# Performance work log

Hardware: AMD Instinct MI355X
Metric: run time of the kernel (lower is better)

Reference implementation:

```python
import jax, jax.numpy as jnp
import numpy as np

N_NODES = 100000


def gcn_conv(x, W, b, src, dst, n):
    # x: [N, Fin], W: [Fin, Fout]. GCNConv: D^-1/2 (A+I) D^-1/2 (X W) + b
    h = x @ W  # [N, Fout]
    ones = jnp.ones_like(dst, dtype=h.dtype)
    deg = jax.ops.segment_sum(ones, dst, num_segments=n)  # in-degree incl self-loops
    dinv = jnp.where(deg > 0, jax.lax.rsqrt(deg), 0.0)
    norm = dinv[src] * dinv[dst]  # [E]
    msg = h[src] * norm[:, None]  # gather + scale
    out = jax.ops.segment_sum(msg, dst, num_segments=n)  # scatter-add
    return out + b


def setup_inputs() -> dict:
    key = jax.random.key(0)
    k1, k2, k3, k4 = jax.random.split(key, 4)
    F_IN, H, C, E = 512, 256, 40, 3200000
    x = jax.random.normal(k1, (N_NODES, F_IN), dtype=jnp.float32)
    # glorot-ish init
    W1 = jax.random.normal(k2, (F_IN, H), dtype=jnp.float32) * (1.0 / np.sqrt(F_IN))
    b1 = jnp.zeros((H,), dtype=jnp.float32)
    W2 = jax.random.normal(k3, (H, C), dtype=jnp.float32) * (1.0 / np.sqrt(H))
    b2 = jnp.zeros((C,), dtype=jnp.float32)
    edge_index = jax.random.randint(k4, (2, E), 0, N_NODES, dtype=jnp.int64)
    return {"x": x, "W1": W1, "b1": b1, "W2": W2, "b2": b2, "edge_index": edge_index}


def reference(x, W1, b1, W2, b2, edge_index):
    n = x.shape[0]
    # add self-loops (PyG GCNConv default add_self_loops=True)
    loop = jnp.arange(n, dtype=edge_index.dtype)
    src = jnp.concatenate([edge_index[0], loop])
    dst = jnp.concatenate([edge_index[1], loop])
    h = gcn_conv(x, W1, b1, src, dst, n)
    h = jax.nn.relu(h)
    # F.dropout(training=self.training): identity in eval mode
    h = gcn_conv(h, W2, b2, src, dst, n)
    return jax.nn.log_softmax(h, axis=1)
```

## Files before the change

kernel.cpp:

```cpp
#include <hip/hip_runtime.h>
#include <stdint.h>

typedef __attribute__((ext_vector_type(8))) short bf16x8;
typedef __attribute__((ext_vector_type(4))) float f32x4;
typedef __attribute__((ext_vector_type(4))) int i32x4;

__device__ __forceinline__ unsigned short f2bf(float f) {
    unsigned int u = __float_as_uint(f);
    u += 0x7FFFu + ((u >> 16) & 1u);
    return (unsigned short)(u >> 16);
}
__device__ __forceinline__ float bf2f(unsigned short s) {
    return __uint_as_float(((unsigned int)s) << 16);
}
__device__ __forceinline__ unsigned char fp8_enc(float f) {
    f = fminf(fmaxf(f, -448.f), 448.f);
    unsigned int u = __float_as_uint(f * 0x1p-120f);
    u += 0x7FFFFu + ((u >> 20) & 1u);
    return (unsigned char)(((u >> 20) & 0x7F) | ((u >> 24) & 0x80));
}

#define SLAB_CAP 5120

__global__ __launch_bounds__(256) void k_bscatter(const int* __restrict__ src,
                                                  const int* __restrict__ dst, int E,
                                                  int* __restrict__ bcnt,
                                                  int* __restrict__ slab, int nbuck) {
    __shared__ int lh[1024];
    __shared__ int lcur[1024];
    const int CH = 8192;
    int e0 = blockIdx.x * CH;
    int e1 = min(E, e0 + CH);
    for (int i = threadIdx.x; i < nbuck; i += 256) lh[i] = 0;
    __syncthreads();
    for (int i = e0 + threadIdx.x; i < e1; i += 256) atomicAdd(&lh[dst[i] >> 7], 1);
    __syncthreads();
    for (int i = threadIdx.x; i < nbuck; i += 256) {
        int c = lh[i];
        lh[i] = c ? atomicAdd(&bcnt[i], c) : 0;
        lcur[i] = 0;
    }
    __syncthreads();
    for (int i = e0 + threadIdx.x; i < e1; i += 256) {
        int d = dst[i], s = src[i];
        int b = d >> 7;
        int p = lh[b] + atomicAdd(&lcur[b], 1);
        if (p < SLAB_CAP) slab[(size_t)b * SLAB_CAP + p] = ((d & 127) << 20) | s;
    }
}

__global__ __launch_bounds__(1024) void k_bscan(const int* __restrict__ bcnt,
                                                int* __restrict__ bbase, int nbuck) {
    __shared__ int sh[1024];
    int t = threadIdx.x;
    int v = (t < nbuck) ? min(bcnt[t], SLAB_CAP) : 0;
    sh[t] = v;
    __syncthreads();
    for (int off = 1; off < 1024; off <<= 1) {
        int x = (t >= off) ? sh[t - off] : 0;
        __syncthreads();
        sh[t] += x;
        __syncthreads();
    }
    if (t < nbuck) bbase[t] = sh[t] - v;
    if (t == 1023) bbase[nbuck] = sh[1023];
}

__global__ __launch_bounds__(256) void k_bcsr(const int* __restrict__ slab,
                                              const int* __restrict__ bcnt,
                                              const int* __restrict__ bbase,
                                              int* __restrict__ rowp,
                                              int* __restrict__ col,
                                              float* __restrict__ dinv, int n, int nbuck) {
    __shared__ int lh[128], lsc[128], lcur[128];
    const int b = blockIdx.x;
    const int base = bbase[b];
    const int cnt = min(bcnt[b], SLAB_CAP);
    const int t = threadIdx.x;
    const int* sl = slab + (size_t)b * SLAB_CAP;
    if (t < 128) lh[t] = 0;
    __syncthreads();
    for (int i = t; i < cnt; i += 256) atomicAdd(&lh[sl[i] >> 20], 1);
    __syncthreads();
    if (t < 128) lsc[t] = lh[t];
    __syncthreads();
    for (int off = 1; off < 128; off <<= 1) {
        int x = (t < 128 && t >= off) ? lsc[t - off] : 0;
        __syncthreads();
        if (t < 128) lsc[t] += x;
        __syncthreads();
    }
    if (t < 128) {
        int excl = lsc[t] - lh[t];
        lcur[t] = excl;
        int v = (b << 7) + t;
        if (v < n) {
            rowp[v] = base + excl;
            dinv[v] = rsqrtf((float)lh[t] + 1.0f);
        }
    }
    if (b == 0 && t == 0) rowp[n] = bbase[nbuck];
    __syncthreads();
    for (int i = t; i < cnt; i += 256) {
        int pk = sl[i];
        int d = pk >> 20;
        int p = base + atomicAdd(&lcur[d], 1);
        col[p] = pk & 0xFFFFF;
    }
}

__global__ __launch_bounds__(256) void k_cvt_w(const float* __restrict__ W1,
                                               const float* __restrict__ W2,
                                               short* __restrict__ W1t,
                                               short* __restrict__ W2t,
                                               int n1, int n2) {
    int i = blockIdx.x * blockDim.x + threadIdx.x;
    if (i < n1) {
        int k = i >> 8, c = i & 255;
        W1t[(size_t)c * 512 + k] = (short)f2bf(W1[i]);
    } else if (i < n1 + n2) {
        int i2 = i - n1;
        int k = i2 / 40, c = i2 - k * 40;
        W2t[(size_t)c * 256 + k] = (short)f2bf(W2[i2]);
    }
}

__global__ __launch_bounds__(512) void k_gemm1(const float* __restrict__ A,
                                               const short* __restrict__ Bt,
                                               const float* __restrict__ dinv,
                                               unsigned char* __restrict__ outp, int M) {
    const int K = 512;
    __shared__ __align__(16) short As[128 * 32];
    __shared__ __align__(16) short Bs[256 * 32];
    const int tid = threadIdx.x;
    const int m0 = blockIdx.x * 128;
    const int w = tid >> 6, lane = tid & 63;
    const int quad = lane >> 4, l16 = lane & 15;
    const int mbase = (w >> 2) * 64, nbase = (w & 3) * 64;

    f32x4 acc[4][4];
#pragma unroll
    for (int i = 0; i < 4; i++)
#pragma unroll
        for (int j = 0; j < 4; j++) acc[i][j] = (f32x4){0.f, 0.f, 0.f, 0.f};

    for (int k0 = 0; k0 < K; k0 += 32) {
#pragma unroll
        for (int s = tid; s < 1024; s += 512) {
            int r = s >> 3, seg = s & 7;
            int gr = m0 + r;
            if (gr >= M) gr = M - 1;
            float4 v = *(const float4*)(A + (size_t)gr * K + k0 + seg * 4);
            ushort4 o;
            o.x = f2bf(v.x); o.y = f2bf(v.y); o.z = f2bf(v.z); o.w = f2bf(v.w);
            *(ushort4*)(As + r * 32 + seg * 4) = o;
        }
#pragma unroll
        for (int s = tid; s < 1024; s += 512) {
            int r = s >> 2, seg = s & 3;
            i32x4 v = *(const i32x4*)(Bt + (size_t)r * K + k0 + seg * 8);
            *(i32x4*)(Bs + r * 32 + seg * 8) = v;
        }
        __syncthreads();
        bf16x8 af[4], bfr[4];
#pragma unroll
        for (int i = 0; i < 4; i++)
            af[i] = *(const bf16x8*)(As + (mbase + i * 16 + l16) * 32 + quad * 8);
#pragma unroll
        for (int j = 0; j < 4; j++)
            bfr[j] = *(const bf16x8*)(Bs + (nbase + j * 16 + l16) * 32 + quad * 8);
#pragma unroll
        for (int i = 0; i < 4; i++)
#pragma unroll
            for (int j = 0; j < 4; j++)
                acc[i][j] = __builtin_amdgcn_mfma_f32_16x16x32_bf16(af[i], bfr[j], acc[i][j], 0, 0, 0);
        __syncthreads();
    }

#pragma unroll
    for (int i = 0; i < 4; i++) {
#pragma unroll
        for (int r = 0; r < 4; r++) {
            int row = m0 + mbase + i * 16 + quad * 4 + r;
            if (row < M) {
                float dv = dinv[row] * 64.f;
#pragma unroll
                for (int j = 0; j < 4; j++)
                    outp[(size_t)row * 256 + nbase + j * 16 + l16] =
                        fp8_enc(acc[i][j][r] * dv);
            }
        }
    }
}

__global__ __launch_bounds__(256) void k_gemm2(const short* __restrict__ A,
                                               const short* __restrict__ Bt,
                                               const float* __restrict__ dinv,
                                               unsigned char* __restrict__ outp, int M) {
    const int K = 256;
    __shared__ __align__(16) short As[128 * 32];
    __shared__ __align__(16) short Bs[64 * 32];
    const int tid = threadIdx.x;
    const int m0 = blockIdx.x * 128;
    const int w = tid >> 6, lane = tid & 63;
    const int quad = lane >> 4, l16 = lane & 15;
    const int mbase = (w >> 1) * 64, nbase = (w & 1) * 32;

    f32x4 acc[4][2];
#pragma unroll
    for (int i = 0; i < 4; i++)
#pragma unroll
        for (int j = 0; j < 2; j++) acc[i][j] = (f32x4){0.f, 0.f, 0.f, 0.f};

    for (int k0 = 0; k0 < K; k0 += 32) {
#pragma unroll
        for (int s = tid; s < 512; s += 256) {
            int r = s >> 2, seg = s & 3;
            int gr = m0 + r;
            if (gr >= M) gr = M - 1;
            i32x4 v = *(const i32x4*)(A + (size_t)gr * K + k0 + seg * 8);
            *(i32x4*)(As + r * 32 + seg * 8) = v;
        }
        if (tid < 256) {
            int r = tid >> 2, seg = tid & 3;
            i32x4 v = *(const i32x4*)(Bt + (size_t)r * K + k0 + seg * 8);
            *(i32x4*)(Bs + r * 32 + seg * 8) = v;
        }
        __syncthreads();
        bf16x8 af[4], bfr[2];
#pragma unroll
        for (int i = 0; i < 4; i++)
            af[i] = *(const bf16x8*)(As + (mbase + i * 16 + l16) * 32 + quad * 8);
#pragma unroll
        for (int j = 0; j < 2; j++)
            bfr[j] = *(const bf16x8*)(Bs + (nbase + j * 16 + l16) * 32 + quad * 8);
#pragma unroll
        for (int i = 0; i < 4; i++)
#pragma unroll
            for (int j = 0; j < 2; j++)
                acc[i][j] = __builtin_amdgcn_mfma_f32_16x16x32_bf16(af[i], bfr[j], acc[i][j], 0, 0, 0);
        __syncthreads();
    }

#pragma unroll
    for (int i = 0; i < 4; i++) {
#pragma unroll
        for (int r = 0; r < 4; r++) {
            int row = m0 + mbase + i * 16 + quad * 4 + r;
            if (row < M) {
                float dv = dinv[row] * 64.f;
#pragma unroll
                for (int j = 0; j < 2; j++)
                    outp[(size_t)row * 64 + nbase + j * 16 + l16] =
                        fp8_enc(acc[i][j][r] * dv);
            }
        }
    }
}

__global__ __launch_bounds__(256) void k_agg1(const unsigned char* __restrict__ h1p,
                                              const int* __restrict__ rowp,
                                              const int* __restrict__ col,
                                              const float* __restrict__ dinv,
                                              const float* __restrict__ b1,
                                              short* __restrict__ h2, int n) {
    const unsigned int* __restrict__ hw = (const unsigned int*)h1p;
    const int w = threadIdx.x >> 6, lane = threadIdx.x & 63;
    const int v = blockIdx.x * 4 + w;
    if (v >= n) return;
    float a0, a1, a2, a3;
    {
        unsigned int u = hw[(size_t)v * 64 + lane];
        a0 = __builtin_amdgcn_cvt_f32_fp8(u, 0);
        a1 = __builtin_amdgcn_cvt_f32_fp8(u, 1);
        a2 = __builtin_amdgcn_cvt_f32_fp8(u, 2);
        a3 = __builtin_amdgcn_cvt_f32_fp8(u, 3);
    }
    const int e0 = rowp[v], e1 = rowp[v + 1];
    int e = e0;
    for (; e + 4 <= e1; e += 4) {
        int s0 = col[e], s1 = col[e + 1], s2 = col[e + 2], s3 = col[e + 3];
        unsigned int u0 = hw[(size_t)s0 * 64 + lane];
        unsigned int u1 = hw[(size_t)s1 * 64 + lane];
        unsigned int u2 = hw[(size_t)s2 * 64 + lane];
        unsigned int u3 = hw[(size_t)s3 * 64 + lane];
        a0 += __builtin_amdgcn_cvt_f32_fp8(u0, 0) + __builtin_amdgcn_cvt_f32_fp8(u1, 0)
            + __builtin_amdgcn_cvt_f32_fp8(u2, 0) + __builtin_amdgcn_cvt_f32_fp8(u3, 0);
        a1 += __builtin_amdgcn_cvt_f32_fp8(u0, 1) + __builtin_amdgcn_cvt_f32_fp8(u1, 1)
            + __builtin_amdgcn_cvt_f32_fp8(u2, 1) + __builtin_amdgcn_cvt_f32_fp8(u3, 1);
        a2 += __builtin_amdgcn_cvt_f32_fp8(u0, 2) + __builtin_amdgcn_cvt_f32_fp8(u1, 2)
            + __builtin_amdgcn_cvt_f32_fp8(u2, 2) + __builtin_amdgcn_cvt_f32_fp8(u3, 2);
        a3 += __builtin_amdgcn_cvt_f32_fp8(u0, 3) + __builtin_amdgcn_cvt_f32_fp8(u1, 3)
            + __builtin_amdgcn_cvt_f32_fp8(u2, 3) + __builtin_amdgcn_cvt_f32_fp8(u3, 3);
    }
    for (; e < e1; e++) {
        unsigned int u = hw[(size_t)col[e] * 64 + lane];
        a0 += __builtin_amdgcn_cvt_f32_fp8(u, 0);
        a1 += __builtin_amdgcn_cvt_f32_fp8(u, 1);
        a2 += __builtin_amdgcn_cvt_f32_fp8(u, 2);
        a3 += __builtin_amdgcn_cvt_f32_fp8(u, 3);
    }
    const int c4 = lane * 4;
    const float dv = dinv[v] * 0x1p-6f;
    float r0 = fmaxf(fmaf(dv, a0, b1[c4 + 0]), 0.f);
    float r1 = fmaxf(fmaf(dv, a1, b1[c4 + 1]), 0.f);
    float r2 = fmaxf(fmaf(dv, a2, b1[c4 + 2]), 0.f);
    float r3 = fmaxf(fmaf(dv, a3, b1[c4 + 3]), 0.f);
    ushort4 o;
    o.x = f2bf(r0); o.y = f2bf(r1); o.z = f2bf(r2); o.w = f2bf(r3);
    *(ushort4*)(h2 + (size_t)v * 256 + c4) = o;
}

__global__ __launch_bounds__(256) void k_agg2(const unsigned char* __restrict__ zp,
                                              const int* __restrict__ rowp,
                                              const int* __restrict__ col,
                                              const float* __restrict__ dinv,
                                              const float* __restrict__ b2,
                                              float* __restrict__ out, int n) {
    const unsigned int* __restrict__ zw = (const unsigned int*)zp;
    const int w = threadIdx.x >> 6, lane = threadIdx.x & 63;
    const int g = lane >> 4, sl = lane & 15;
    const int v = blockIdx.x * 16 + w * 4 + g;
    if (v >= n) return;
    float a0, a1, a2, a3;
    {
        unsigned int u = zw[(size_t)v * 16 + sl];
        a0 = __builtin_amdgcn_cvt_f32_fp8(u, 0);
        a1 = __builtin_amdgcn_cvt_f32_fp8(u, 1);
        a2 = __builtin_amdgcn_cvt_f32_fp8(u, 2);
        a3 = __builtin_amdgcn_cvt_f32_fp8(u, 3);
    }
    const int e0 = rowp[v], e1 = rowp[v + 1];
    int e = e0;
    for (; e + 4 <= e1; e += 4) {
        int s0 = col[e], s1 = col[e + 1], s2 = col[e + 2], s3 = col[e + 3];
        unsigned int u0 = zw[(size_t)s0 * 16 + sl];
        unsigned int u1 = zw[(size_t)s1 * 16 + sl];
        unsigned int u2 = zw[(size_t)s2 * 16 + sl];
        unsigned int u3 = zw[(size_t)s3 * 16 + sl];
        a0 += __builtin_amdgcn_cvt_f32_fp8(u0, 0) + __builtin_amdgcn_cvt_f32_fp8(u1, 0)
            + __builtin_amdgcn_cvt_f32_fp8(u2, 0) + __builtin_amdgcn_cvt_f32_fp8(u3, 0);
        a1 += __builtin_amdgcn_cvt_f32_fp8(u0, 1) + __builtin_amdgcn_cvt_f32_fp8(u1, 1)
            + __builtin_amdgcn_cvt_f32_fp8(u2, 1) + __builtin_amdgcn_cvt_f32_fp8(u3, 1);
        a2 += __builtin_amdgcn_cvt_f32_fp8(u0, 2) + __builtin_amdgcn_cvt_f32_fp8(u1, 2)
            + __builtin_amdgcn_cvt_f32_fp8(u2, 2) + __builtin_amdgcn_cvt_f32_fp8(u3, 2);
        a3 += __builtin_amdgcn_cvt_f32_fp8(u0, 3) + __builtin_amdgcn_cvt_f32_fp8(u1, 3)
            + __builtin_amdgcn_cvt_f32_fp8(u2, 3) + __builtin_amdgcn_cvt_f32_fp8(u3, 3);
    }
    for (; e < e1; e++) {
        unsigned int u = zw[(size_t)col[e] * 16 + sl];
        a0 += __builtin_amdgcn_cvt_f32_fp8(u, 0);
        a1 += __builtin_amdgcn_cvt_f32_fp8(u, 1);
        a2 += __builtin_amdgcn_cvt_f32_fp8(u, 2);
        a3 += __builtin_amdgcn_cvt_f32_fp8(u, 3);
    }
    const int f = sl * 4;
    const float dv = dinv[v] * 0x1p-6f;
    float l0 = (f + 0 < 40) ? fmaf(dv, a0, b2[f + 0]) : -1e30f;
    float l1 = (f + 1 < 40) ? fmaf(dv, a1, b2[f + 1]) : -1e30f;
    float l2 = (f + 2 < 40) ? fmaf(dv, a2, b2[f + 2]) : -1e30f;
    float l3 = (f + 3 < 40) ? fmaf(dv, a3, b2[f + 3]) : -1e30f;
    float m = fmaxf(fmaxf(l0, l1), fmaxf(l2, l3));
    m = fmaxf(m, __shfl_xor(m, 1));
    m = fmaxf(m, __shfl_xor(m, 2));
    m = fmaxf(m, __shfl_xor(m, 4));
    m = fmaxf(m, __shfl_xor(m, 8));
    float es = expf(l0 - m) + expf(l1 - m) + expf(l2 - m) + expf(l3 - m);
    es += __shfl_xor(es, 1);
    es += __shfl_xor(es, 2);
    es += __shfl_xor(es, 4);
    es += __shfl_xor(es, 8);
    float ls = m + logf(es);
    if (sl < 10) {
        float4 o = {l0 - ls, l1 - ls, l2 - ls, l3 - ls};
        *(float4*)(out + (size_t)v * 40 + f) = o;
    }
}

extern "C" void kernel_launch(void* const* d_in, const int* in_sizes, int n_in,
                              void* d_out, int out_size, void* d_ws, size_t ws_size,
                              hipStream_t stream) {
    const float* x  = (const float*)d_in[0];
    const float* W1 = (const float*)d_in[1];
    const float* b1 = (const float*)d_in[2];
    const float* W2 = (const float*)d_in[3];
    const float* b2 = (const float*)d_in[4];
    const int*   ei = (const int*)d_in[5];
    float* out = (float*)d_out;

    const int FIN = 512, H = 256, C = 40;
    const int n = in_sizes[0] / FIN;
    const int E = in_sizes[5] / 2;
    const int nbuck = (n + 127) >> 7;

    auto align_up = [](size_t v) { return (v + 255) & ~(size_t)255; };
    char* base = (char*)d_ws;
    size_t off = 0;
    unsigned char* h1p = (unsigned char*)(base + off); off += align_up((size_t)n * H);
    short* h2    = (short*)(base + off); off += align_up((size_t)n * H * 2);
    unsigned char* zp = (unsigned char*)(base + off); off += align_up((size_t)n * 64);
    float* dinv  = (float*)(base + off); off += align_up((size_t)n * 4);
    int* rowp    = (int*)(base + off);   off += align_up((size_t)(n + 1) * 4);
    int* colarr  = (int*)(base + off);   off += align_up((size_t)E * 4);
    int* slab    = (int*)(base + off);   off += align_up((size_t)nbuck * SLAB_CAP * 4);
    short* W1t   = (short*)(base + off); off += align_up((size_t)H * FIN * 2);
    short* W2t   = (short*)(base + off); off += align_up((size_t)64 * H * 2);
    int* bcnt    = (int*)(base + off);   off += align_up((size_t)(nbuck + 1) * 4);
    int* bbase   = (int*)(base + off);   off += align_up((size_t)(nbuck + 1) * 4);

    const int* srcp = ei;
    const int* dstp = ei + E;

    hipMemsetAsync(bcnt, 0, (size_t)(nbuck + 1) * 4, stream);
    hipMemsetAsync(W2t, 0, (size_t)64 * H * 2, stream);

    k_bscatter<<<(E + 8191) / 8192, 256, 0, stream>>>(srcp, dstp, E, bcnt, slab, nbuck);
    k_bscan<<<1, 1024, 0, stream>>>(bcnt, bbase, nbuck);
    k_bcsr<<<nbuck, 256, 0, stream>>>(slab, bcnt, bbase, rowp, colarr, dinv, n, nbuck);

    int n1 = FIN * H, n2 = H * C;
    k_cvt_w<<<(n1 + n2 + 255) / 256, 256, 0, stream>>>(W1, W2, W1t, W2t, n1, n2);

    k_gemm1<<<(n + 127) / 128, 512, 0, stream>>>(x, W1t, dinv, h1p, n);
    k_agg1<<<(n + 3) / 4, 256, 0, stream>>>(h1p, rowp, colarr, dinv, b1, h2, n);

    k_gemm2<<<(n + 127) / 128, 256, 0, stream>>>(h2, W2t, dinv, zp, n);
    k_agg2<<<(n + 15) / 16, 256, 0, stream>>>(zp, rowp, colarr, dinv, b2, out, n);
}
```

Baseline: 638.7 us.

## Split agg1 edges across lane groups with 16-byte gathers and packed fp8 conversion

The layer-1 aggregation is restructured. Each wave splits its node's edges across four 16-lane groups, and each lane gathers 16 fp8 bytes with one vector load instead of 4 bytes. Partial sums are combined with cross-group shuffles. Both aggregation kernels use the packed fp8-to-f32x2 conversion builtin, and agg2 unrolls its edge loop to 8. This aims to cut load instruction count and raise memory-level parallelism in the gather-bound aggregation, at the cost of more registers and shuffle reductions.

```diff
diff --git a/kernel.cpp b/kernel.cpp
--- a/kernel.cpp
+++ b/kernel.cpp
@@ -4,6 +4,9 @@
 typedef __attribute__((ext_vector_type(8))) short bf16x8;
 typedef __attribute__((ext_vector_type(4))) float f32x4;
 typedef __attribute__((ext_vector_type(4))) int i32x4;
+typedef __attribute__((ext_vector_type(2))) float f32x2;
+typedef __attribute__((ext_vector_type(4))) unsigned int u32x4;
+typedef __attribute__((ext_vector_type(8))) unsigned short ushort8_t;
 
 __device__ __forceinline__ unsigned short f2bf(float f) {
     unsigned int u = __float_as_uint(f);
@@ -18,6 +21,29 @@
     unsigned int u = __float_as_uint(f * 0x1p-120f);
     u += 0x7FFFFu + ((u >> 20) & 1u);
     return (unsigned char)(((u >> 20) & 0x7F) | ((u >> 24) & 0x80));
+}
+
+__device__ __forceinline__ f32x2 cvtpk0(unsigned int u) {
+#if __has_builtin(__builtin_amdgcn_cvt_pk_f32_fp8)
+    auto r = __builtin_amdgcn_cvt_pk_f32_fp8((int)u, false);
+    f32x2 o; o.x = r[0]; o.y = r[1]; return o;
+#else
+    f32x2 o;
+    o.x = __builtin_amdgcn_cvt_f32_fp8(u, 0);
+    o.y = __builtin_amdgcn_cvt_f32_fp8(u, 1);
+    return o;
+#endif
+}
+__device__ __forceinline__ f32x2 cvtpk1(unsigned int u) {
+#if __has_builtin(__builtin_amdgcn_cvt_pk_f32_fp8)
+    auto r = __builtin_amdgcn_cvt_pk_f32_fp8((int)u, true);
+    f32x2 o; o.x = r[0]; o.y = r[1]; return o;
+#else
+    f32x2 o;
+    o.x = __builtin_amdgcn_cvt_f32_fp8(u, 2);
+    o.y = __builtin_amdgcn_cvt_f32_fp8(u, 3);
+    return o;
+#endif
 }
 
 #define SLAB_CAP 5120
@@ -264,51 +290,75 @@
                                               const float* __restrict__ dinv,
                                               const float* __restrict__ b1,
                                               short* __restrict__ h2, int n) {
-    const unsigned int* __restrict__ hw = (const unsigned int*)h1p;
+    const u32x4* __restrict__ hq = (const u32x4*)h1p;
     const int w = threadIdx.x >> 6, lane = threadIdx.x & 63;
+    const int g = lane >> 4, sl = lane & 15;
     const int v = blockIdx.x * 4 + w;
     if (v >= n) return;
-    float a0, a1, a2, a3;
+
+    f32x2 acc[8];
     {
-        unsigned int u = hw[(size_t)v * 64 + lane];
-        a0 = __builtin_amdgcn_cvt_f32_fp8(u, 0);
-        a1 = __builtin_amdgcn_cvt_f32_fp8(u, 1);
-        a2 = __builtin_amdgcn_cvt_f32_fp8(u, 2);
-        a3 = __builtin_amdgcn_cvt_f32_fp8(u, 3);
-    }
+        u32x4 q = (u32x4){0u, 0u, 0u, 0u};
+        if (g == 0) q = hq[(size_t)v * 16 + sl];
+#pragma unroll
+        for (int i = 0; i < 4; i++) {
+            acc[2 * i] = cvtpk0(q[i]);
+            acc[2 * i + 1] = cvtpk1(q[i]);
+        }
+    }
+
     const int e0 = rowp[v], e1 = rowp[v + 1];
-    int e = e0;
-    for (; e + 4 <= e1; e += 4) {
-        int s0 = col[e], s1 = col[e + 1], s2 = col[e + 2], s3 = col[e + 3];
-        unsigned int u0 = hw[(size_t)s0 * 64 + lane];
-        unsigned int u1 = hw[(size_t)s1 * 64 + lane];
-        unsigned int u2 = hw[(size_t)s2 * 64 + lane];
-        unsigned int u3 = hw[(size_t)s3 * 64 + lane];
-        a0 += __builtin_amdgcn_cvt_f32_fp8(u0, 0) + __builtin_amdgcn_cvt_f32_fp8(u1, 0)
-            + __builtin_amdgcn_cvt_f32_fp8(u2, 0) + __builtin_amdgcn_cvt_f32_fp8(u3, 0);
-        a1 += __builtin_amdgcn_cvt_f32_fp8(u0, 1) + __builtin_amdgcn_cvt_f32_fp8(u1, 1)
-            + __builtin_amdgcn_cvt_f32_fp8(u2, 1) + __builtin_amdgcn_cvt_f32_fp8(u3, 1);
-        a2 += __builtin_amdgcn_cvt_f32_fp8(u0, 2) + __builtin_amdgcn_cvt_f32_fp8(u1, 2)
-            + __builtin_amdgcn_cvt_f32_fp8(u2, 2) + __builtin_amdgcn_cvt_f32_fp8(u3, 2);
-        a3 += __builtin_amdgcn_cvt_f32_fp8(u0, 3) + __builtin_amdgcn_cvt_f32_fp8(u1, 3)
-            + __builtin_amdgcn_cvt_f32_fp8(u2, 3) + __builtin_amdgcn_cvt_f32_fp8(u3, 3);
-    }
-    for (; e < e1; e++) {
-        unsigned int u = hw[(size_t)col[e] * 64 + lane];
-        a0 += __builtin_amdgcn_cvt_f32_fp8(u, 0);
-        a1 += __builtin_amdgcn_cvt_f32_fp8(u, 1);
-        a2 += __builtin_amdgcn_cvt_f32_fp8(u, 2);
-        a3 += __builtin_amdgcn_cvt_f32_fp8(u, 3);
-    }
-    const int c4 = lane * 4;
-    const float dv = dinv[v] * 0x1p-6f;
-    float r0 = fmaxf(fmaf(dv, a0, b1[c4 + 0]), 0.f);
-    float r1 = fmaxf(fmaf(dv, a1, b1[c4 + 1]), 0.f);
-    float r2 = fmaxf(fmaf(dv, a2, b1[c4 + 2]), 0.f);
-    float r3 = fmaxf(fmaf(dv, a3, b1[c4 + 3]), 0.f);
-    ushort4 o;
-    o.x = f2bf(r0); o.y = f2bf(r1); o.z = f2bf(r2); o.w = f2bf(r3);
-    *(ushort4*)(h2 + (size_t)v * 256 + c4) = o;
+    const int nedge = e1 - e0;
+    const int full = nedge & ~7;
+    for (int t = 0; t < full; t += 8) {
+        int ea = e0 + t + g;
+        int sa = col[ea], sb = col[ea + 4];
+        u32x4 qa = hq[(size_t)sa * 16 + sl];
+        u32x4 qb = hq[(size_t)sb * 16 + sl];
+#pragma unroll
+        for (int i = 0; i < 4; i++) {
+            acc[2 * i] += cvtpk0(qa[i]);
+            acc[2 * i + 1] += cvtpk1(qa[i]);
+        }
+#pragma unroll
+        for (int i = 0; i < 4; i++) {
+            acc[2 * i] += cvtpk0(qb[i]);
+            acc[2 * i + 1] += cvtpk1(qb[i]);
+        }
+    }
+    for (int t = full + g; t < nedge; t += 4) {
+        u32x4 q = hq[(size_t)col[e0 + t] * 16 + sl];
+#pragma unroll
+        for (int i = 0; i < 4; i++) {
+            acc[2 * i] += cvtpk0(q[i]);
+            acc[2 * i + 1] += cvtpk1(q[i]);
+        }
+    }
+
+#pragma unroll
+    for (int i = 0; i < 8; i++) {
+        acc[i].x += __shfl_xor(acc[i].x, 16);
+        acc[i].y += __shfl_xor(acc[i].y, 16);
+        acc[i].x += __shfl_xor(acc[i].x, 32);
+        acc[i].y += __shfl_xor(acc[i].y, 32);
+    }
+
+    if (g < 2) {
+        const float dv = dinv[v] * 0x1p-6f;
+        const float4* bq = (const float4*)(b1 + sl * 16 + g * 8);
+        ushort8_t o;
+#pragma unroll
+        for (int k = 0; k < 2; k++) {
+            float4 bb = bq[k];
+            f32x2 p0 = acc[g * 4 + k * 2];
+            f32x2 p1 = acc[g * 4 + k * 2 + 1];
+            o[k * 4 + 0] = f2bf(fmaxf(fmaf(dv, p0.x, bb.x), 0.f));
+            o[k * 4 + 1] = f2bf(fmaxf(fmaf(dv, p0.y, bb.y), 0.f));
+            o[k * 4 + 2] = f2bf(fmaxf(fmaf(dv, p1.x, bb.z), 0.f));
+            o[k * 4 + 3] = f2bf(fmaxf(fmaf(dv, p1.y, bb.w), 0.f));
+        }
+        *(ushort8_t*)(h2 + (size_t)v * 256 + sl * 16 + g * 8) = o;
+    }
 }
 
 __global__ __launch_bounds__(256) void k_agg2(const unsigned char* __restrict__ zp,
@@ -322,44 +372,47 @@
     const int g = lane >> 4, sl = lane & 15;
     const int v = blockIdx.x * 16 + w * 4 + g;
     if (v >= n) return;
-    float a0, a1, a2, a3;
+    f32x2 a01, a23;
     {
         unsigned int u = zw[(size_t)v * 16 + sl];
-        a0 = __builtin_amdgcn_cvt_f32_fp8(u, 0);
-        a1 = __builtin_amdgcn_cvt_f32_fp8(u, 1);
-        a2 = __builtin_amdgcn_cvt_f32_fp8(u, 2);
-        a3 = __builtin_amdgcn_cvt_f32_fp8(u, 3);
+        a01 = cvtpk0(u);
+        a23 = cvtpk1(u);
     }
     const int e0 = rowp[v], e1 = rowp[v + 1];
     int e = e0;
-    for (; e + 4 <= e1; e += 4) {
+    for (; e + 8 <= e1; e += 8) {
         int s0 = col[e], s1 = col[e + 1], s2 = col[e + 2], s3 = col[e + 3];
+        int s4 = col[e + 4], s5 = col[e + 5], s6 = col[e + 6], s7 = col[e + 7];
         unsigned int u0 = zw[(size_t)s0 * 16 + sl];
         unsigned int u1 = zw[(size_t)s1 * 16 + sl];
         unsigned int u2 = zw[(size_t)s2 * 16 + sl];
         unsigned int u3 = zw[(size_t)s3 * 16 + sl];
-        a0 += __builtin_amdgcn_cvt_f32_fp8(u0, 0) + __builtin_amdgcn_cvt_f32_fp8(u1, 0)
-            + __builtin_amdgcn_cvt_f32_fp8(u2, 0) + __builtin_amdgcn_cvt_f32_fp8(u3, 0);
-        a1 += __builtin_amdgcn_cvt_f32_fp8(u0, 1) + __builtin_amdgcn_cvt_f32_fp8(u1, 1)
-            + __builtin_amdgcn_cvt_f32_fp8(u2, 1) + __builtin_amdgcn_cvt_f32_fp8(u3, 1);
-        a2 += __builtin_amdgcn_cvt_f32_fp8(u0, 2) + __builtin_amdgcn_cvt_f32_fp8(u1, 2)
-            + __builtin_amdgcn_cvt_f32_fp8(u2, 2) + __builtin_amdgcn_cvt_f32_fp8(u3, 2);
-        a3 += __builtin_amdgcn_cvt_f32_fp8(u0, 3) + __builtin_amdgcn_cvt_f32_fp8(u1, 3)
-            + __builtin_amdgcn_cvt_f32_fp8(u2, 3) + __builtin_amdgcn_cvt_f32_fp8(u3, 3);
+        unsigned int u4 = zw[(size_t)s4 * 16 + sl];
+        unsigned int u5 = zw[(size_t)s5 * 16 + sl];
+        unsigned int u6 = zw[(size_t)s6 * 16 + sl];
+        unsigned int u7 = zw[(size_t)s7 * 16 + sl];
+        a01 += cvtpk0(u0) + cvtpk0(u1) + cvtpk0(u2) + cvtpk0(u3)
+             + cvtpk0(u4) + cvtpk0(u5) + cvtpk0(u6) + cvtpk0(u7);
+        a23 += cvtpk1(u0) + cvtpk1(u1) + cvtpk1(u2) + cvtpk1(u3)
+             + cvtpk1(u4) + cvtpk1(u5) + cvtpk1(u6) + cvtpk1(u7);
+    }
+    for (; e + 2 <= e1; e += 2) {
+        unsigned int u0 = zw[(size_t)col[e] * 16 + sl];
+        unsigned int u1 = zw[(size_t)col[e + 1] * 16 + sl];
+        a01 += cvtpk0(u0) + cvtpk0(u1);
+        a23 += cvtpk1(u0) + cvtpk1(u1);
     }
     for (; e < e1; e++) {
         unsigned int u = zw[(size_t)col[e] * 16 + sl];
-        a0 += __builtin_amdgcn_cvt_f32_fp8(u, 0);
-        a1 += __builtin_amdgcn_cvt_f32_fp8(u, 1);
-        a2 += __builtin_amdgcn_cvt_f32_fp8(u, 2);
-        a3 += __builtin_amdgcn_cvt_f32_fp8(u, 3);
+        a01 += cvtpk0(u);
+        a23 += cvtpk1(u);
     }
     const int f = sl * 4;
     const float dv = dinv[v] * 0x1p-6f;
-    float l0 = (f + 0 < 40) ? fmaf(dv, a0, b2[f + 0]) : -1e30f;
-    float l1 = (f + 1 < 40) ? fmaf(dv, a1, b2[f + 1]) : -1e30f;
-    float l2 = (f + 2 < 40) ? fmaf(dv, a2, b2[f + 2]) : -1e30f;
-    float l3 = (f + 3 < 40) ? fmaf(dv, a3, b2[f + 3]) : -1e30f;
+    float l0 = (f + 0 < 40) ? fmaf(dv, a01.x, b2[f + 0]) : -1e30f;
+    float l1 = (f + 1 < 40) ? fmaf(dv, a01.y, b2[f + 1]) : -1e30f;
+    float l2 = (f + 2 < 40) ? fmaf(dv, a23.x, b2[f + 2]) : -1e30f;
+    float l3 = (f + 3 < 40) ? fmaf(dv, a23.y, b2[f + 3]) : -1e30f;
     float m = fmaxf(fmaxf(l0, l1), fmaxf(l2, l3));
     m = fmaxf(m, __shfl_xor(m, 1));
     m = fmaxf(m, __shfl_xor(m, 2));
```

Result: no change. 632.8 us (median of 2 runs) (-0.9%).
